# Kernel tuning notes

Measured on AMD Instinct MI355X. Metric: run time of the kernel, lower is better.

## Reference

```python
import jax, jax.numpy as jnp
import numpy as np

FP4_E2M1_VALUES = [0.0, 0.0625, 8.0, 1.0, 2.0, 3.0, 4.0, 6.0,
                   -0.0, -0.0625, -8.0, -1.0, -2.0, -3.0, -4.0, -6.0]

M, N, K = 4096, 4096, 4096


def setup_inputs() -> dict:
    key = jax.random.key(0)
    k1, k2 = jax.random.split(key)
    x = jax.random.normal(k1, (M, K), dtype=jnp.float16)
    # packed uint8 bytes stored as int32 (values in [0,256)); each byte holds
    # two fp4 indices: high nibble = even k, low nibble = odd k
    packed_weight = jax.random.randint(k2, (N, K // 2), 0, 256, dtype=jnp.int32)
    lut = jnp.array(FP4_E2M1_VALUES, dtype=jnp.float16)
    return {"x": x, "packed_weight": packed_weight, "lut": lut}


def reference(x, packed_weight, lut):
    # Dequantize: unpack nibbles along K, LUT lookup -> W [N, K] fp16
    n, kh = packed_weight.shape
    high = (packed_weight >> 4) & 15   # even k positions
    low = packed_weight & 15           # odd k positions
    idx = jnp.stack([high, low], axis=-1).reshape(n, 2 * kh)  # [N, K]
    w = lut[idx]                       # [N, K] fp16
    # GEMM with fp32 accumulation (Triton kernel accumulates in fp32), cast to fp16
    y = jnp.einsum('mk,nk->mn', x, w, preferred_element_type=jnp.float32)
    return y.astype(jnp.float16)
```

## Files before the change

kernel.cpp:

```cpp
#include <hip/hip_runtime.h>
#include <hip/hip_fp16.h>
#include <stdint.h>

#define M_DIM 4096
#define N_DIM 4096
#define K_DIM 4096
#define KW (K_DIM / 2)
#define WS_XH_BYTES ((size_t)M_DIM * K_DIM * 2)
#define WS_WH_BYTES ((size_t)N_DIM * K_DIM * 2)

typedef _Float16 half8 __attribute__((ext_vector_type(8)));
typedef float f32x4 __attribute__((ext_vector_type(4)));

__device__ __forceinline__ uint32_t pk2(float a, float b) {
  auto h = __builtin_amdgcn_cvt_pkrtz(a, b);
  return __builtin_bit_cast(uint32_t, h);
}

__device__ __forceinline__ uint32_t dq(uint32_t b, uint32_t ph, uint32_t pl) {
#if __has_builtin(__builtin_amdgcn_perm)
  const uint32_t sel = ((b & 0x70u) << 4) | ((b & 0x07u) << 24);
  uint32_t v = __builtin_amdgcn_perm(ph, pl, sel);
#else
  const uint64_t pool = ((uint64_t)ph << 32) | pl;
  const uint32_t mh = (uint32_t)(pool >> (((b >> 4) & 7u) * 8)) & 0xFFu;
  const uint32_t ml = (uint32_t)(pool >> ((b & 7u) * 8)) & 0xFFu;
  uint32_t v = (mh << 8) | (ml << 24);
#endif
  const uint32_t sg = ((b & 0x88u) * 0x10000100u) & 0x80008000u;
  return v | sg;
}

__device__ __forceinline__ void lut_pool(const float* __restrict__ lutf,
                                         uint32_t& ph, uint32_t& pl) {
  const uint32_t h01 = pk2(lutf[0], lutf[1]);
  const uint32_t h23 = pk2(lutf[2], lutf[3]);
  const uint32_t h45 = pk2(lutf[4], lutf[5]);
  const uint32_t h67 = pk2(lutf[6], lutf[7]);
#if __has_builtin(__builtin_amdgcn_perm)
  pl = __builtin_amdgcn_perm(h23, h01, 0x07050301u);
  ph = __builtin_amdgcn_perm(h67, h45, 0x07050301u);
#else
  pl = ((h01 >> 8) & 0xFFu) | ((h01 >> 24) << 8) |
       (((h23 >> 8) & 0xFFu) << 16) | ((h23 >> 24) << 24);
  ph = ((h45 >> 8) & 0xFFu) | ((h45 >> 24) << 8) |
       (((h67 >> 8) & 0xFFu) << 16) | ((h67 >> 24) << 24);
#endif
}

#define XBLOCKS (M_DIM * K_DIM / 8 / 256)
#define WBLOCKS (N_DIM * KW / 4 / 256)

__global__ __launch_bounds__(256) void prep_kernel(
    const float4* __restrict__ xin, uint4* __restrict__ xout,
    const int4* __restrict__ pin, uint4* __restrict__ wout,
    const float* __restrict__ lutf) {
  const int b = blockIdx.x;
  if (b < XBLOCKS) {
    const int i = b * 256 + threadIdx.x;
    const float4 v0 = xin[2 * i];
    const float4 v1 = xin[2 * i + 1];
    xout[i] = make_uint4(pk2(v0.x, v0.y), pk2(v0.z, v0.w),
                         pk2(v1.x, v1.y), pk2(v1.z, v1.w));
  } else {
    uint32_t ph, pl;
    lut_pool(lutf, ph, pl);
    const int i = (b - XBLOCKS) * 256 + threadIdx.x;
    const int4 w = pin[i];
    wout[i] = make_uint4(dq(w.x, ph, pl), dq(w.y, ph, pl),
                         dq(w.z, ph, pl), dq(w.w, ph, pl));
  }
}

__global__ __launch_bounds__(256) void cvt_x_kernel(const float4* __restrict__ xin,
                                                    uint4* __restrict__ xout) {
  const int i = blockIdx.x * 256 + threadIdx.x;
  const float4 v0 = xin[2 * i];
  const float4 v1 = xin[2 * i + 1];
  xout[i] = make_uint4(pk2(v0.x, v0.y), pk2(v0.z, v0.w),
                       pk2(v1.x, v1.y), pk2(v1.z, v1.w));
}

__device__ __forceinline__ f32x4 mfma16(half8 a, half8 b, f32x4 c) {
  return __builtin_amdgcn_mfma_f32_16x16x32_f16(a, b, c, 0, 0, 0);
}

#define NT (K_DIM / 64)

__global__ __launch_bounds__(512, 2) void f16gemm256_kernel(
    const uint8_t* __restrict__ xh,
    const uint8_t* __restrict__ wh,
    float* __restrict__ out)
{
  __shared__ uint16_t Al[2][2][256 * 32];
  __shared__ uint16_t Bl[2][2][256 * 32];

  const int tid  = threadIdx.x;
  const int lane = tid & 63;
  const int wave = tid >> 6;
  const int wm   = wave >> 2;
  const int wn   = wave & 3;

  const int bid = blockIdx.x;
  const int sw  = (bid & 7) * 32 + (bid >> 3);
  const int m0  = (sw >> 4) * 256;
  const int n0  = (sw & 15) * 256;

  const uint8_t* asrc[2];
  const uint8_t* bsrc[2];
  int ldst[2];
#pragma unroll
  for (int s = 0; s < 2; ++s) {
    const int slot = tid + s * 512;
    const int row  = slot >> 2;
    const int g    = (slot & 3) ^ ((row >> 1) & 3);
    asrc[s] = xh + ((size_t)(m0 + row) * K_DIM) * 2 + g * 16;
    bsrc[s] = wh + ((size_t)(n0 + row) * K_DIM) * 2 + g * 16;
    ldst[s] = slot * 16;
  }

  auto STAGE = [&](int isB, int buf, int kh, int tt) {
    const int koff  = tt * 128 + kh * 64;
    uint8_t* lb = (uint8_t*)(isB ? &Bl[0][0][0] : &Al[0][0][0]) +
                  (buf * 2 + kh) * 16384;
#pragma unroll
    for (int s = 0; s < 2; ++s) {
      const uint8_t* gp = (isB ? bsrc[s] : asrc[s]) + koff;
      __builtin_amdgcn_global_load_lds(
          (const __attribute__((address_space(1))) uint32_t*)gp,
          (__attribute__((address_space(3))) uint32_t*)(lb + ldst[s]), 16, 0, 0);
    }
  };

  int aoff[8], boff[4];
#pragma unroll
  for (int m = 0; m < 8; ++m) {
    const int row = wm * 128 + m * 16 + (lane & 15);
    const int ch  = (lane >> 4) ^ ((row >> 1) & 3);
    aoff[m] = row * 32 + ch * 8;
  }
#pragma unroll
  for (int n = 0; n < 4; ++n) {
    const int row = wn * 64 + n * 16 + (lane & 15);
    const int ch  = (lane >> 4) ^ ((row >> 1) & 3);
    boff[n] = row * 32 + ch * 8;
  }

  f32x4 acc[8][4];
#pragma unroll
  for (int i = 0; i < 8; ++i)
#pragma unroll
    for (int j = 0; j < 4; ++j) acc[i][j] = (f32x4){0.f, 0.f, 0.f, 0.f};

  STAGE(1, 0, 0, 0);
  STAGE(0, 0, 0, 0);
  STAGE(1, 0, 1, 0);
  STAGE(0, 0, 1, 0);
  STAGE(1, 1, 0, 1);
  STAGE(0, 1, 0, 1);
  asm volatile("s_waitcnt vmcnt(8)" ::: "memory");
  __builtin_amdgcn_s_barrier();

  half8 af[8], bfr[4];

#pragma unroll 2
  for (int t = 0; t < NT; ++t) {
    const int cur = t & 1;
    const uint16_t* Ab = &Al[cur][0][0];
    const uint16_t* Bb = &Bl[cur][0][0];
    const bool st1 = (t + 1 < NT);
    const bool st2 = (t + 2 < NT);

    __builtin_amdgcn_s_setprio(1);
#pragma unroll
    for (int n = 0; n < 4; ++n) bfr[n] = *(const half8*)(Bb + boff[n]);
#pragma unroll
    for (int m = 0; m < 8; ++m) af[m] = *(const half8*)(Ab + aoff[m]);
    if (st1) { STAGE(1, cur ^ 1, 1, t + 1); STAGE(0, cur ^ 1, 1, t + 1); }
#pragma unroll
    for (int m = 0; m < 8; ++m)
#pragma unroll
      for (int n = 0; n < 4; ++n)
        acc[m][n] = mfma16(af[m], bfr[n], acc[m][n]);
    __builtin_amdgcn_s_setprio(0);
    if (st1) asm volatile("s_waitcnt vmcnt(8)" ::: "memory");
    else     asm volatile("s_waitcnt vmcnt(0)" ::: "memory");
    __builtin_amdgcn_s_barrier();

    __builtin_amdgcn_s_setprio(1);
#pragma unroll
    for (int n = 0; n < 4; ++n) bfr[n] = *(const half8*)(Bb + 8192 + boff[n]);
#pragma unroll
    for (int m = 0; m < 8; ++m) af[m] = *(const half8*)(Ab + 8192 + aoff[m]);
    if (st2) { STAGE(1, cur, 0, t + 2); STAGE(0, cur, 0, t + 2); }
#pragma unroll
    for (int m = 0; m < 8; ++m)
#pragma unroll
      for (int n = 0; n < 4; ++n)
        acc[m][n] = mfma16(af[m], bfr[n], acc[m][n]);
    __builtin_amdgcn_s_setprio(0);
    if (st2)      asm volatile("s_waitcnt vmcnt(8)" ::: "memory");
    else if (st1) asm volatile("s_waitcnt vmcnt(4)" ::: "memory");
    __builtin_amdgcn_s_barrier();
  }

  const int mb = m0 + wm * 128 + (lane >> 4) * 4;
  const int nb = n0 + wn * 64 + (lane & 15);
#pragma unroll
  for (int m = 0; m < 8; ++m)
#pragma unroll
    for (int n = 0; n < 4; ++n)
#pragma unroll
      for (int r = 0; r < 4; ++r)
        out[(size_t)(mb + m * 16 + r) * N_DIM + (nb + n * 16)] = acc[m][n][r];
}

#define BM 128
#define BN 128
#define BK 32

__global__ __launch_bounds__(256, 2) void fp4gemm_kernel(
    const uint8_t* __restrict__ xh, const int* __restrict__ pw,
    const float* __restrict__ lutf, float* __restrict__ out)
{
  __shared__ uint16_t ldsA[BM * BK];
  __shared__ uint16_t ldsB[BN * BK];

  const int tid  = threadIdx.x;
  const int lane = tid & 63;
  const int wave = tid >> 6;
  const int wm   = wave >> 1;
  const int wn   = wave & 1;
  const int m0 = blockIdx.y * BM;
  const int n0 = blockIdx.x * BN;

  uint32_t ph, pl;
  lut_pool(lutf, ph, pl);

  f32x4 acc[4][4];
#pragma unroll
  for (int i = 0; i < 4; ++i)
#pragma unroll
    for (int j = 0; j < 4; ++j) acc[i][j] = (f32x4){0.f, 0.f, 0.f, 0.f};

  const int rowB  = tid >> 1;
  const int halfB = tid & 1;
  const int swzB  = (rowB >> 1) & 3;

  for (int kt = 0; kt < K_DIM / BK; ++kt) {
    __syncthreads();

#pragma unroll
    for (int s = 0; s < 2; ++s) {
      const int idx = tid + s * 256;
      const int row = idx >> 2;
      const int c16 = idx & 3;
      const int g16 = c16 ^ ((row >> 1) & 3);
      const uint8_t* gp = xh + ((size_t)(m0 + row) * K_DIM + kt * BK) * 2 + g16 * 16;
      uint8_t* lp = (uint8_t*)ldsA + (size_t)idx * 16;
      __builtin_amdgcn_global_load_lds(
          (const __attribute__((address_space(1))) uint32_t*)gp,
          (__attribute__((address_space(3))) uint32_t*)lp, 16, 0, 0);
    }

    {
      const int* gp = pw + (size_t)(n0 + rowB) * KW + kt * (BK / 2) + halfB * 8;
      const int4 wA = ((const int4*)gp)[0];
      const int4 wB = ((const int4*)gp)[1];
      uint8_t* base = (uint8_t*)ldsB + rowB * 64;
      *(uint4*)(base + ((halfB * 2 + 0) ^ swzB) * 16) =
          make_uint4(dq(wA.x, ph, pl), dq(wA.y, ph, pl),
                     dq(wA.z, ph, pl), dq(wA.w, ph, pl));
      *(uint4*)(base + ((halfB * 2 + 1) ^ swzB) * 16) =
          make_uint4(dq(wB.x, ph, pl), dq(wB.y, ph, pl),
                     dq(wB.z, ph, pl), dq(wB.w, ph, pl));
    }

    __syncthreads();

    const int q = lane >> 4;
    half8 af[4], bfr[4];
#pragma unroll
    for (int i = 0; i < 4; ++i) {
      const int row = wm * 64 + i * 16 + (lane & 15);
      af[i] = *(const half8*)(ldsA + row * BK + (q ^ ((row >> 1) & 3)) * 8);
    }
#pragma unroll
    for (int j = 0; j < 4; ++j) {
      const int row = wn * 64 + j * 16 + (lane & 15);
      bfr[j] = *(const half8*)(ldsB + row * BK + (q ^ ((row >> 1) & 3)) * 8);
    }
#pragma unroll
    for (int i = 0; i < 4; ++i)
#pragma unroll
      for (int j = 0; j < 4; ++j)
        acc[i][j] = __builtin_amdgcn_mfma_f32_16x16x32_f16(af[i], bfr[j], acc[i][j], 0, 0, 0);
  }

  const int mb = m0 + wm * 64 + (lane >> 4) * 4;
  const int nb = n0 + wn * 64 + (lane & 15);
#pragma unroll
  for (int i = 0; i < 4; ++i)
#pragma unroll
    for (int j = 0; j < 4; ++j)
#pragma unroll
      for (int r = 0; r < 4; ++r)
        out[(size_t)(mb + i * 16 + r) * N_DIM + (nb + j * 16)] = acc[i][j][r];
}

extern "C" void kernel_launch(void* const* d_in, const int* in_sizes, int n_in,
                              void* d_out, int out_size, void* d_ws, size_t ws_size,
                              hipStream_t stream) {
  const void* px = nullptr; const void* ppw = nullptr; const void* plut = nullptr;
  for (int i = 0; i < n_in; ++i) {
    const long s = in_sizes[i];
    if (s == (long)M_DIM * K_DIM) px = d_in[i];
    else if (s == (long)N_DIM * KW) ppw = d_in[i];
    else if (s == 16) plut = d_in[i];
  }
  if (!px || !ppw || !plut) { px = d_in[0]; ppw = d_in[1]; plut = d_in[2]; }

  if (ws_size >= WS_XH_BYTES + WS_WH_BYTES) {
    uint8_t* wh = (uint8_t*)d_ws + WS_XH_BYTES;
    prep_kernel<<<XBLOCKS + WBLOCKS, 256, 0, stream>>>(
        (const float4*)px, (uint4*)d_ws, (const int4*)ppw, (uint4*)wh,
        (const float*)plut);
    f16gemm256_kernel<<<dim3(256), dim3(512), 0, stream>>>(
        (const uint8_t*)d_ws, wh, (float*)d_out);
  } else {
    cvt_x_kernel<<<(M_DIM * K_DIM / 8) / 256, 256, 0, stream>>>(
        (const float4*)px, (uint4*)d_ws);
    dim3 grid(N_DIM / BN, M_DIM / BM);
    fp4gemm_kernel<<<grid, dim3(256), 0, stream>>>(
        (const uint8_t*)d_ws, (const int*)ppw, (const float*)plut, (float*)d_out);
  }
}
```

Before: 254.0 us.

## Double-buffer LDS fragment registers to overlap reads with MFMA

Splits the A/B fragment registers into two sets so that the LDS reads for the next half-tile are issued before the MFMAs run on the current set, with sched_barrier keeping the compiler from reordering them. The vmcnt waits and the prologue are adjusted so fragments for the next K-tile load right after the barrier. The aim is to hide LDS read latency behind matrix math. The cost is higher register pressure from holding 24 extra half8 registers, which could lower occupancy or cause spills. The changed waitcnt logic also risks reading LDS before the data has arrived.

```diff
diff --git a/kernel.cpp b/kernel.cpp
--- a/kernel.cpp
+++ b/kernel.cpp
@@ -161,46 +161,63 @@
   asm volatile("s_waitcnt vmcnt(8)" ::: "memory");
   __builtin_amdgcn_s_barrier();
 
-  half8 af[8], bfr[4];
+  half8 afA[8], bfA[4];
+  half8 afB[8], bfB[4];
+
+  {
+    const uint16_t* Ab = &Al[0][0][0];
+    const uint16_t* Bb = &Bl[0][0][0];
+#pragma unroll
+    for (int n = 0; n < 4; ++n) bfA[n] = *(const half8*)(Bb + boff[n]);
+#pragma unroll
+    for (int m = 0; m < 8; ++m) afA[m] = *(const half8*)(Ab + aoff[m]);
+  }
+  asm volatile("s_waitcnt vmcnt(4)" ::: "memory");
+  __builtin_amdgcn_s_barrier();
 
 #pragma unroll 2
   for (int t = 0; t < NT; ++t) {
     const int cur = t & 1;
-    const uint16_t* Ab = &Al[cur][0][0];
-    const uint16_t* Bb = &Bl[cur][0][0];
+    const uint16_t* Ab  = &Al[cur][0][0];
+    const uint16_t* Bb  = &Bl[cur][0][0];
+    const uint16_t* Ab2 = &Al[cur ^ 1][0][0];
+    const uint16_t* Bb2 = &Bl[cur ^ 1][0][0];
     const bool st1 = (t + 1 < NT);
     const bool st2 = (t + 2 < NT);
 
     __builtin_amdgcn_s_setprio(1);
 #pragma unroll
-    for (int n = 0; n < 4; ++n) bfr[n] = *(const half8*)(Bb + boff[n]);
-#pragma unroll
-    for (int m = 0; m < 8; ++m) af[m] = *(const half8*)(Ab + aoff[m]);
+    for (int n = 0; n < 4; ++n) bfB[n] = *(const half8*)(Bb + 8192 + boff[n]);
+#pragma unroll
+    for (int m = 0; m < 8; ++m) afB[m] = *(const half8*)(Ab + 8192 + aoff[m]);
     if (st1) { STAGE(1, cur ^ 1, 1, t + 1); STAGE(0, cur ^ 1, 1, t + 1); }
+    __builtin_amdgcn_sched_barrier(0);
 #pragma unroll
     for (int m = 0; m < 8; ++m)
 #pragma unroll
       for (int n = 0; n < 4; ++n)
-        acc[m][n] = mfma16(af[m], bfr[n], acc[m][n]);
+        acc[m][n] = mfma16(afA[m], bfA[n], acc[m][n]);
     __builtin_amdgcn_s_setprio(0);
-    if (st1) asm volatile("s_waitcnt vmcnt(8)" ::: "memory");
-    else     asm volatile("s_waitcnt vmcnt(0)" ::: "memory");
+    if (st1) asm volatile("s_waitcnt vmcnt(4)" ::: "memory");
     __builtin_amdgcn_s_barrier();
 
     __builtin_amdgcn_s_setprio(1);
-#pragma unroll
-    for (int n = 0; n < 4; ++n) bfr[n] = *(const half8*)(Bb + 8192 + boff[n]);
-#pragma unroll
-    for (int m = 0; m < 8; ++m) af[m] = *(const half8*)(Ab + 8192 + aoff[m]);
+    if (st1) {
+#pragma unroll
+      for (int n = 0; n < 4; ++n) bfA[n] = *(const half8*)(Bb2 + boff[n]);
+#pragma unroll
+      for (int m = 0; m < 8; ++m) afA[m] = *(const half8*)(Ab2 + aoff[m]);
+    }
     if (st2) { STAGE(1, cur, 0, t + 2); STAGE(0, cur, 0, t + 2); }
+    __builtin_amdgcn_sched_barrier(0);
 #pragma unroll
     for (int m = 0; m < 8; ++m)
 #pragma unroll
       for (int n = 0; n < 4; ++n)
-        acc[m][n] = mfma16(af[m], bfr[n], acc[m][n]);
+        acc[m][n] = mfma16(afB[m], bfB[n], acc[m][n]);
     __builtin_amdgcn_s_setprio(0);
-    if (st2)      asm volatile("s_waitcnt vmcnt(8)" ::: "memory");
-    else if (st1) asm volatile("s_waitcnt vmcnt(4)" ::: "memory");
+    if (st2)      asm volatile("s_waitcnt vmcnt(4)" ::: "memory");
+    else if (st1) asm volatile("s_waitcnt vmcnt(0)" ::: "memory");
     __builtin_amdgcn_s_barrier();
   }
 
```

Result: slower. 509.5 us (+100.6%).
